# Kernel optimization log

Hardware: AMD Instinct MI355X
Metric: run time of the kernel (lower is better)

## Reference

```python
import jax, jax.numpy as jnp
import numpy as np

HIDDEN = 4096
N_HEADS = 32
N_KV_HEADS = 8
HEAD_DIM = HIDDEN // N_HEADS  # 128
N_GROUPS = N_HEADS // N_KV_HEADS  # 4
ROPE_THETA = 10000.0
BSZ, SEQ = 2, 2048


def rotate_half(x):
    x1 = x[..., : x.shape[-1] // 2]
    x2 = x[..., x.shape[-1] // 2 :]
    return jnp.concatenate((-x2, x1), axis=-1)


def rope_tables(seq_len, head_dim, theta):
    inv_freq = 1.0 / theta ** (jnp.arange(0, head_dim, 2, dtype=jnp.float32) / head_dim)
    t = jnp.arange(seq_len, dtype=jnp.float32)
    freqs = jnp.einsum('i,j->ij', t, inv_freq)          # [S, head_dim/2]
    emb = jnp.concatenate((freqs, freqs), axis=-1)       # [S, head_dim]
    return jnp.cos(emb), jnp.sin(emb)


def setup_inputs() -> dict:
    key = jax.random.key(0)
    ks = jax.random.split(key, 5)
    hidden_states = jax.random.normal(ks[0], (BSZ, SEQ, HIDDEN), dtype=jnp.float32)
    # causal additive mask [B, 1, Q, K]
    causal = jnp.tril(jnp.ones((SEQ, SEQ), dtype=bool))
    attention_mask = jnp.where(causal, 0.0, -1e9).astype(jnp.float32)
    attention_mask = jnp.broadcast_to(attention_mask[None, None], (BSZ, 1, SEQ, SEQ))
    position_ids = jnp.broadcast_to(jnp.arange(SEQ, dtype=jnp.int32)[None, :], (BSZ, SEQ))
    sc = 1.0 / np.sqrt(HIDDEN)
    Wq = jax.random.normal(ks[1], (HIDDEN, N_HEADS * HEAD_DIM), dtype=jnp.float32) * sc
    Wk = jax.random.normal(ks[2], (HIDDEN, N_KV_HEADS * HEAD_DIM), dtype=jnp.float32) * sc
    Wv = jax.random.normal(ks[3], (HIDDEN, N_KV_HEADS * HEAD_DIM), dtype=jnp.float32) * sc
    Wo = jax.random.normal(ks[4], (N_HEADS * HEAD_DIM, HIDDEN), dtype=jnp.float32) * sc
    return {
        'hidden_states': hidden_states,
        'attention_mask': attention_mask,
        'position_ids': position_ids,
        'Wq': Wq, 'Wk': Wk, 'Wv': Wv, 'Wo': Wo,
    }


def reference(hidden_states, attention_mask, position_ids, Wq, Wk, Wv, Wo):
    bsz, q_len, _ = hidden_states.shape
    # QKV projections
    q = (hidden_states @ Wq).reshape(bsz, q_len, N_HEADS, HEAD_DIM).swapaxes(1, 2)       # [B,H,S,D]
    k = (hidden_states @ Wk).reshape(bsz, q_len, N_KV_HEADS, HEAD_DIM).swapaxes(1, 2)    # [B,Hkv,S,D]
    v = (hidden_states @ Wv).reshape(bsz, q_len, N_KV_HEADS, HEAD_DIM).swapaxes(1, 2)    # [B,Hkv,S,D]
    # RoPE
    cos_t, sin_t = rope_tables(q_len, HEAD_DIM, ROPE_THETA)
    cos = jnp.take(cos_t, position_ids, axis=0)[:, None]  # [B,1,S,D]
    sin = jnp.take(sin_t, position_ids, axis=0)[:, None]
    q = q * cos + rotate_half(q) * sin
    k = k * cos + rotate_half(k) * sin
    # GQA attention via grouped einsum (equivalent to repeat_kv, without materializing repeats)
    qg = q.reshape(bsz, N_KV_HEADS, N_GROUPS, q_len, HEAD_DIM)
    scores = jnp.einsum('bhgqd,bhkd->bhgqk', qg, k) / jnp.sqrt(jnp.float32(HEAD_DIM))
    scores = scores + attention_mask[:, :, None]  # broadcast mask over (kv_head, group)
    probs = jax.nn.softmax(scores.astype(jnp.float32), axis=-1).astype(hidden_states.dtype)
    out = jnp.einsum('bhgqk,bhkd->bhgqd', probs, v)
    out = out.reshape(bsz, N_HEADS, q_len, HEAD_DIM).swapaxes(1, 2).reshape(bsz, q_len, HIDDEN)
    return out @ Wo
```

## Files before the change

kernel.cpp:

```cpp
#include <hip/hip_runtime.h>
#include <hip/hip_bf16.h>
#include <cstdint>

#define HIDDEN 4096
#define NH 32
#define NKV 8
#define HD 128
#define SEQ 2048
#define BSZ 2
#define QKVN 6144
#define QKVLD 6144

using bf16x8 = __attribute__((ext_vector_type(8))) short;
using f32x4  = __attribute__((ext_vector_type(4))) float;
using f32x16 = __attribute__((ext_vector_type(16))) float;

__device__ __forceinline__ ushort f2bf(float f) {
  union { float f; uint32_t u; } v; v.f = f;
  uint32_t r = (v.u + 0x7FFFu + ((v.u >> 16) & 1u)) >> 16;
  return (ushort)r;
}
__device__ __forceinline__ float bf2f(ushort s) {
  union { uint32_t u; float f; } v; v.u = ((uint32_t)s) << 16;
  return v.f;
}

__device__ __forceinline__ uint32_t cvtpk(float lo, float hi) {
  uint32_t r;
  asm("v_cvt_pk_bf16_f32 %0, %1, %2" : "=v"(r) : "v"(lo), "v"(hi));
  return r;
}
__device__ __forceinline__ void pl32swap(uint32_t& a, uint32_t& b) {
  asm("v_permlane32_swap_b32 %0, %1" : "+v"(a), "+v"(b));
}

__device__ __forceinline__ void gload_lds16(const void* g, void* l) {
  __builtin_amdgcn_global_load_lds(
      (const __attribute__((address_space(1))) void*)g,
      (__attribute__((address_space(3))) void*)l, 16, 0, 0);
}

__global__ __launch_bounds__(256)
void cvt_bf16_kernel(const float* __restrict__ X, ushort* __restrict__ Xb, int n8) {
  int t = blockIdx.x * 256 + threadIdx.x;
  if (t >= n8) return;
  size_t i = (size_t)t * 8;
  float4 a = *(const float4*)(X + i);
  float4 b = *(const float4*)(X + i + 4);
  uint4 p;
  p.x = (uint)f2bf(a.x) | ((uint)f2bf(a.y) << 16);
  p.y = (uint)f2bf(a.z) | ((uint)f2bf(a.w) << 16);
  p.z = (uint)f2bf(b.x) | ((uint)f2bf(b.y) << 16);
  p.w = (uint)f2bf(b.z) | ((uint)f2bf(b.w) << 16);
  *(uint4*)(Xb + i) = p;
}

__global__ __launch_bounds__(256)
void transpose_bf16_kernel(const float* __restrict__ W, ushort* __restrict__ WT,
                           int K, int N) {
  __shared__ ushort tile[64][72];
  const int k0 = blockIdx.y * 64, n0 = blockIdx.x * 64;
  const int tr = threadIdx.x >> 4;
  const int tc = (threadIdx.x & 15) * 4;
#pragma unroll
  for (int i = 0; i < 4; ++i) {
    const int k = tr + i * 16;
    float4 v = *(const float4*)(W + (size_t)(k0 + k) * N + n0 + tc);
    ushort4 u;
    u.x = f2bf(v.x); u.y = f2bf(v.y); u.z = f2bf(v.z); u.w = f2bf(v.w);
    *(ushort4*)&tile[k][tc] = u;
  }
  __syncthreads();
  const int nr = threadIdx.x >> 3;
  const int kc = (threadIdx.x & 7) * 8;
#pragma unroll
  for (int i = 0; i < 2; ++i) {
    const int n = nr + i * 32;
    bf16x8 o;
#pragma unroll
    for (int j = 0; j < 8; ++j) o[j] = tile[kc + j][n];
    *(bf16x8*)(WT + (size_t)(n0 + n) * K + k0 + kc) = o;
  }
}

__global__ __launch_bounds__(256)
void transpose_v_kernel(const ushort* __restrict__ Vsrc, ushort* __restrict__ VtG) {
  __shared__ ushort tile[64][72];
  const int slice = blockIdx.z;
  const int b = slice >> 3, kh = slice & 7;
  const int s0 = blockIdx.x * 64, d0 = blockIdx.y * 64;
  const ushort* src = Vsrc + ((size_t)(b * SEQ) + s0) * QKVLD + kh * HD + d0;
  const int sr = threadIdx.x >> 3;
  const int dc = (threadIdx.x & 7) * 8;
#pragma unroll
  for (int i = 0; i < 2; ++i) {
    const int s = sr + i * 32;
    *(bf16x8*)&tile[s][dc] = *(const bf16x8*)(src + (size_t)s * QKVLD + dc);
  }
  __syncthreads();
  ushort* dst = VtG + ((size_t)slice * HD + d0) * SEQ + s0;
  const int dr = threadIdx.x >> 3;
  const int sc = (threadIdx.x & 7) * 8;
#pragma unroll
  for (int i = 0; i < 2; ++i) {
    const int d = dr + i * 32;
    bf16x8 o;
#pragma unroll
    for (int j = 0; j < 8; ++j) o[j] = tile[sc + j][d];
    *(bf16x8*)(dst + (size_t)d * SEQ + sc) = o;
  }
}

__global__ __launch_bounds__(512, 2)
void gemmqkv_kernel(const ushort* __restrict__ A, const ushort* __restrict__ BT,
                    ushort* __restrict__ Cp, int M, int N, int K) {
  extern __shared__ ushort lds[];
  const int tid = threadIdx.x, lane = tid & 63, wave = tid >> 6;
  const int l15 = lane & 15, l4 = lane >> 4;
  const int wr = wave >> 2, wc = wave & 3;

  const int mt = M >> 8, ntile = N / 192, nwg = mt * ntile;
  const int swq = nwg >> 3, swr = nwg & 7;
  const int xcd = blockIdx.x & 7, lo = blockIdx.x >> 3;
  const int wg = (xcd < swr ? xcd * (swq + 1) : swr * (swq + 1) + (xcd - swr) * swq) + lo;
  const int m0 = (wg % mt) << 8;
  const int n0 = (wg / mt) * 192;

  ushort* LA[2][2];
  ushort* LB[2][2];
#pragma unroll
  for (int b_ = 0; b_ < 2; ++b_)
#pragma unroll
    for (int s_ = 0; s_ < 2; ++s_) {
      LA[b_][s_] = lds + (b_ * 2 + s_) * 8192;
      LB[b_][s_] = lds + 32768 + (b_ * 2 + s_) * 6144;
    }

  const ushort* Abase = A + (size_t)m0 * K;
  const ushort* Bbase = BT + (size_t)n0 * K;

  const int srow0 = tid >> 2;
  const int scol8 = (((tid & 3) ^ ((srow0 >> 1) & 3)) << 3);
  const int bs1 = tid;
  const int brow1 = bs1 >> 2;
  const int bcol1 = (((bs1 & 3) ^ ((bs1 >> 3) & 3)) << 3);
  const int bs2 = 512 + wave * 32 + (lane & 31);
  const int brow2 = bs2 >> 2;
  const int bcol2 = (((bs2 & 3) ^ ((bs2 >> 3) & 3)) << 3);

  const int swb  = (l4 ^ ((l15 >> 1) & 3)) << 3;
  const int aoff = (wr * 128 + l15) * 32 + swb;
  const int boff = (wc * 48 + l15) * 32 + swb;

  f32x4 acc[8][3] = {};
  bf16x8 a[4];
  bf16x8 b[3];

#define STAGE_EV(buf, ks, kt)                                                  \
  do {                                                                         \
    const size_t gc_ = (size_t)(kt) * 64 + (ks) * 32;                          \
    gload_lds16(Abase + (size_t)srow0 * K + gc_ + scol8,                       \
                &LA[buf][ks][tid * 8]);                                        \
    gload_lds16(Bbase + (size_t)brow1 * K + gc_ + bcol1,                       \
                &LB[buf][ks][tid * 8]);                                        \
  } while (0)

#define STAGE_OD(buf, ks, kt)                                                  \
  do {                                                                         \
    const size_t gc_ = (size_t)(kt) * 64 + (ks) * 32;                          \
    gload_lds16(Abase + (size_t)(128 + srow0) * K + gc_ + scol8,               \
                &LA[buf][ks][(512 + tid) * 8]);                                \
    if ((lane & 32) == 0)                                                      \
      gload_lds16(Bbase + (size_t)brow2 * K + gc_ + bcol2,                     \
                  &LB[buf][ks][(512 + wave * 32 + (lane & 31)) * 8]);          \
  } while (0)

#define MFMA_ __builtin_amdgcn_mfma_f32_16x16x32_bf16

#define PHASE_EVEN(buf, ks, sb, sk, skt)                                       \
  {                                                                            \
    _Pragma("unroll") for (int m_ = 0; m_ < 4; ++m_)                           \
      a[m_] = *(const bf16x8*)&LA[buf][ks][aoff + m_ * 512];                   \
    _Pragma("unroll") for (int n_ = 0; n_ < 3; ++n_)                           \
      b[n_] = *(const bf16x8*)&LB[buf][ks][boff + n_ * 512];                   \
    STAGE_EV(sb, sk, skt);                                                     \
    asm volatile("s_barrier" ::: "memory");                                    \
    __builtin_amdgcn_s_setprio(1);                                             \
    _Pragma("unroll") for (int m_ = 0; m_ < 4; ++m_)                           \
      _Pragma("unroll") for (int n_ = 0; n_ < 3; ++n_)                         \
        acc[m_][n_] = MFMA_(a[m_], b[n_], acc[m_][n_], 0, 0, 0);               \
    __builtin_amdgcn_s_setprio(0);                                             \
    asm volatile("s_barrier" ::: "memory");                                    \
  }

#define PHASE_ODD(buf, ks, sb, sk, skt)                                        \
  {                                                                            \
    _Pragma("unroll") for (int m_ = 0; m_ < 4; ++m_)                           \
      a[m_] = *(const bf16x8*)&LA[buf][ks][aoff + (4 + m_) * 512];             \
    STAGE_OD(sb, sk, skt);                                                     \
    asm volatile("s_barrier" ::: "memory");                                    \
    __builtin_amdgcn_s_setprio(1);                                             \
    _Pragma("unroll") for (int m_ = 0; m_ < 4; ++m_)                           \
      _Pragma("unroll") for (int n_ = 0; n_ < 3; ++n_)                         \
        acc[4 + m_][n_] = MFMA_(a[m_], b[n_], acc[4 + m_][n_], 0, 0, 0);       \
    __builtin_amdgcn_s_setprio(0);                                             \
    asm volatile("s_waitcnt vmcnt(8)");                                        \
    asm volatile("s_barrier" ::: "memory");                                    \
  }

  const int NT = K >> 6;

  STAGE_EV(0, 0, 0); STAGE_OD(0, 0, 0);
  STAGE_EV(0, 1, 0); STAGE_OD(0, 1, 0);
  STAGE_EV(1, 0, 1); STAGE_OD(1, 0, 1);
  asm volatile("s_waitcnt vmcnt(8)");
  asm volatile("s_barrier" ::: "memory");

  for (int i = 0; i < (NT >> 1); ++i) {
    const int kt0 = 2 * i;
    const int ktA = (kt0 + 2 < NT) ? kt0 + 2 : NT - 1;
    const int ktB = (kt0 + 3 < NT) ? kt0 + 3 : NT - 1;
    PHASE_EVEN(0, 0, 1, 1, kt0 + 1)
    PHASE_ODD (0, 0, 1, 1, kt0 + 1)
    PHASE_EVEN(0, 1, 0, 0, ktA)
    PHASE_ODD (0, 1, 0, 0, ktA)
    PHASE_EVEN(1, 0, 0, 1, ktA)
    PHASE_ODD (1, 0, 0, 1, ktA)
    PHASE_EVEN(1, 1, 1, 0, ktB)
    PHASE_ODD (1, 1, 1, 0, ktB)
  }
#undef PHASE_EVEN
#undef PHASE_ODD
#undef STAGE_EV
#undef STAGE_OD

  const int crow0 = m0 + wr * 128 + l4 * 4;
  const int ccol0 = n0 + wc * 48 + l15;
#pragma unroll
  for (int m_ = 0; m_ < 8; ++m_)
#pragma unroll
    for (int n_ = 0; n_ < 3; ++n_)
#pragma unroll
      for (int r_ = 0; r_ < 4; ++r_) {
        const size_t row = crow0 + m_ * 16 + r_;
        const int col = ccol0 + n_ * 16;
        Cp[row * N + col] = f2bf(acc[m_][n_][r_]);
      }
}

template<int OUT_BF16>
__global__ __launch_bounds__(512, 2)
void gemm8p_kernel(const ushort* __restrict__ A, const ushort* __restrict__ BT,
                   void* __restrict__ Cp, int M, int N, int K) {
  extern __shared__ ushort lds[];
  const int tid = threadIdx.x, lane = tid & 63, wave = tid >> 6;
  const int l15 = lane & 15, l4 = lane >> 4;
  const int wr = wave >> 2, wc = wave & 3;

  const int mt = M >> 8, nt = N >> 8, nwg = mt * nt;
  const int swq = nwg >> 3, swr = nwg & 7;
  const int xcd = blockIdx.x & 7, lo = blockIdx.x >> 3;
  const int wg = (xcd < swr ? xcd * (swq + 1) : swr * (swq + 1) + (xcd - swr) * swq) + lo;
  const int m0 = (wg % mt) << 8;
  const int n0 = (wg / mt) << 8;

  ushort* LA[2][2];
  ushort* LB[2][2];
#pragma unroll
  for (int b_ = 0; b_ < 2; ++b_)
#pragma unroll
    for (int s_ = 0; s_ < 2; ++s_) {
      LA[b_][s_] = lds + ((b_ * 2 + 0) * 2 + s_) * 8192;
      LB[b_][s_] = lds + ((b_ * 2 + 1) * 2 + s_) * 8192;
    }

  const ushort* Abase = A + (size_t)m0 * K;
  const ushort* Bbase = BT + (size_t)n0 * K;

  const int srow0 = tid >> 2;
  const int scol8 = (((tid & 3) ^ ((srow0 >> 1) & 3)) << 3);

  const int swb  = (l4 ^ ((l15 >> 1) & 3)) << 3;
  const int aoff = (wr * 128 + l15) * 32 + swb;
  const int boff = (wc * 64 + l15) * 32 + swb;

  f32x4 acc[8][4] = {};
  bf16x8 a[8];
  bf16x8 b[4];

#define STAGE(buf, ks, kt, part)                                              \
  do {                                                                        \
    const size_t gc_ = (size_t)(kt) * 64 + (ks) * 32 + scol8;                 \
    const int rw_ = srow0 + (part) * 128;                                     \
    const int dst_ = ((part) * 512 + tid) * 8;                                \
    gload_lds16(Abase + (size_t)rw_ * K + gc_, &LA[buf][ks][dst_]);           \
    gload_lds16(Bbase + (size_t)rw_ * K + gc_, &LB[buf][ks][dst_]);           \
  } while (0)

#define MFMA_ __builtin_amdgcn_mfma_f32_16x16x32_bf16

#define PHASE_EVEN(buf, ks, sb, sk, skt)                                      \
  {                                                                           \
    _Pragma("unroll") for (int m_ = 0; m_ < 8; ++m_)                          \
      a[m_] = *(const bf16x8*)&LA[buf][ks][aoff + m_ * 512];                  \
    b[0] = *(const bf16x8*)&LB[buf][ks][boff];                                \
    b[1] = *(const bf16x8*)&LB[buf][ks][boff + 512];                          \
    STAGE(sb, sk, skt, 0);                                                    \
    asm volatile("s_barrier" ::: "memory");                                   \
    __builtin_amdgcn_s_setprio(1);                                            \
    _Pragma("unroll") for (int m_ = 0; m_ < 8; ++m_) {                        \
      acc[m_][0] = MFMA_(a[m_], b[0], acc[m_][0], 0, 0, 0);                   \
      acc[m_][1] = MFMA_(a[m_], b[1], acc[m_][1], 0, 0, 0);                   \
    }                                                                         \
    __builtin_amdgcn_s_setprio(0);                                            \
    asm volatile("s_barrier" ::: "memory");                                   \
  }

#define PHASE_ODD(buf, ks, sb, sk, skt)                                       \
  {                                                                           \
    b[2] = *(const bf16x8*)&LB[buf][ks][boff + 1024];                         \
    b[3] = *(const bf16x8*)&LB[buf][ks][boff + 1536];                         \
    STAGE(sb, sk, skt, 1);                                                    \
    asm volatile("s_barrier" ::: "memory");                                   \
    __builtin_amdgcn_s_setprio(1);                                            \
    _Pragma("unroll") for (int m_ = 0; m_ < 8; ++m_) {                        \
      acc[m_][2] = MFMA_(a[m_], b[2], acc[m_][2], 0, 0, 0);                   \
      acc[m_][3] = MFMA_(a[m_], b[3], acc[m_][3], 0, 0, 0);                   \
    }                                                                         \
    __builtin_amdgcn_s_setprio(0);                                            \
    asm volatile("s_waitcnt vmcnt(8)");                                       \
    asm volatile("s_barrier" ::: "memory");                                   \
  }

  const int NT = K >> 6;

  STAGE(0, 0, 0, 0); STAGE(0, 0, 0, 1);
  STAGE(0, 1, 0, 0); STAGE(0, 1, 0, 1);
  STAGE(1, 0, 1, 0); STAGE(1, 0, 1, 1);
  asm volatile("s_waitcnt vmcnt(8)");
  asm volatile("s_barrier" ::: "memory");

  for (int i = 0; i < (NT >> 1); ++i) {
    const int kt0 = 2 * i;
    const int ktA = (kt0 + 2 < NT) ? kt0 + 2 : NT - 1;
    const int ktB = (kt0 + 3 < NT) ? kt0 + 3 : NT - 1;
    PHASE_EVEN(0, 0, 1, 1, kt0 + 1)
    PHASE_ODD (0, 0, 1, 1, kt0 + 1)
    PHASE_EVEN(0, 1, 0, 0, ktA)
    PHASE_ODD (0, 1, 0, 0, ktA)
    PHASE_EVEN(1, 0, 0, 1, ktA)
    PHASE_ODD (1, 0, 0, 1, ktA)
    PHASE_EVEN(1, 1, 1, 0, ktB)
    PHASE_ODD (1, 1, 1, 0, ktB)
  }
#undef PHASE_EVEN
#undef PHASE_ODD
#undef STAGE

  const int crow0 = m0 + wr * 128 + l4 * 4;
  const int ccol0 = n0 + wc * 64 + l15;
#pragma unroll
  for (int m_ = 0; m_ < 8; ++m_)
#pragma unroll
    for (int n_ = 0; n_ < 4; ++n_)
#pragma unroll
      for (int r_ = 0; r_ < 4; ++r_) {
        const size_t row = crow0 + m_ * 16 + r_;
        const int col = ccol0 + n_ * 16;
        const float val = acc[m_][n_][r_];
        if (OUT_BF16) ((ushort*)Cp)[row * N + col] = f2bf(val);
        else          ((float*)Cp)[row * N + col]  = val;
      }
}

__global__ __launch_bounds__(256)
void rope_qk_kernel(ushort* qkv, const int* __restrict__ pos_ids, int total) {
  int t = blockIdx.x * 256 + threadIdx.x;
  if (t >= total) return;
  int j = t & 63;
  int rest = t >> 6;
  int hp = rest % 40;
  int bs = rest / 40;
  float pos = (float)pos_ids[bs];
  float inv = exp2f(-(float)j * (13.287712379549449f / 64.0f));
  float ang = pos * inv;
  const float osc = (hp < 32) ? 0.12751731f : 1.0f;
  float c = cosf(ang) * osc, s = sinf(ang) * osc;
  const int col = (hp < 32) ? hp * HD : HIDDEN + (hp - 32) * HD;
  ushort* p = qkv + (size_t)bs * QKVLD + col + j;
  float x1 = bf2f(p[0]), x2 = bf2f(p[64]);
  p[0]  = f2bf(x1 * c - x2 * s);
  p[64] = f2bf(x2 * c + x1 * s);
}

__global__ __launch_bounds__(512)
void attn_kernel(const ushort* __restrict__ Q, const ushort* __restrict__ K0,
                 const ushort* __restrict__ VtG, ushort* __restrict__ AO) {
  __shared__ ushort Ks[64 * 128];
  __shared__ ushort Vs[2][128 * 64];

  const int bid = blockIdx.x;
  const int kh  = bid & 7;
  const int r2  = bid >> 3;
  const int qtB = 7 - (r2 & 7);
  const int hq  = (r2 >> 3) & 3;
  const int b   = r2 >> 5;
  const int h   = kh * 4 + hq;
  const int q0b = qtB * 256;

  const int tid = threadIdx.x, lane = tid & 63, w = tid >> 6;
  const int l31 = lane & 31, hi = lane >> 5;
  const int q0w = q0b + w * 32;

  const size_t bS = (size_t)b * SEQ;
  const ushort* Kb = K0 + bS * QKVLD + kh * HD;
  const ushort* Vb = VtG + (size_t)(b * NKV + kh) * HD * SEQ;

  bf16x8 qf[8];
  {
    const ushort* qp = Q + (bS + q0w + l31) * QKVLD + h * HD + hi * 8;
#pragma unroll
    for (int ds = 0; ds < 8; ++ds) qf[ds] = *(const bf16x8*)(qp + ds * 16);
  }

  f32x16 accO[4] = {};
  float mrow = -1e30f, denom = 0.0f;

  const int nt = qtB * 4 + 4;

  const int j0 = 2 * w, j1 = 2 * w + 1;
  const int kl4 = lane >> 4, ks15 = lane & 15;
  const int vl3 = lane >> 3, vs7 = lane & 7;
  const int kswz = lane & 15;
  const int vswz = lane & 7;

#define KSTAGE(jj, kk0) { const int k_ = (jj) * 4 + kl4;                       \
    gload_lds16(Kb + (size_t)((kk0) + k_) * QKVLD + ((ks15 ^ (k_ & 15)) << 3), \
                &Ks[(jj) * 512 + lane * 8]); }
#define VSTAGE(jj, bb, kk0) { const int d_ = (jj) * 8 + vl3;                   \
    gload_lds16(Vb + (size_t)d_ * SEQ + (kk0) + ((vs7 ^ (d_ & 7)) << 3),       \
                &Vs[bb][(jj) * 512 + lane * 8]); }

  KSTAGE(j0, 0) KSTAGE(j1, 0) VSTAGE(j0, 0, 0) VSTAGE(j1, 0, 0)
  __syncthreads();

  for (int t = 0; t < nt; ++t) {
    const int k0 = t * 64;
    const int cur = t & 1;
    const bool pf = (t + 1 < nt);
    const bool skip = (k0 > q0w + 31);

    f32x16 s0 = {}, s1 = {};
    if (!skip) {
      __builtin_amdgcn_s_setprio(1);
#pragma unroll
      for (int ds = 0; ds < 8; ++ds) {
        const int so = ((ds * 2 + hi) ^ kswz) << 3;
        bf16x8 kf0 = *(const bf16x8*)&Ks[l31 * 128 + so];
        bf16x8 kf1 = *(const bf16x8*)&Ks[(32 + l31) * 128 + so];
        s0 = __builtin_amdgcn_mfma_f32_32x32x16_bf16(kf0, qf[ds], s0, 0, 0, 0);
        s1 = __builtin_amdgcn_mfma_f32_32x32x16_bf16(kf1, qf[ds], s1, 0, 0, 0);
      }
      __builtin_amdgcn_s_setprio(0);
    }
    __syncthreads();

    if (pf) {
      const int kn = k0 + 64;
      KSTAGE(j0, kn) KSTAGE(j1, kn) VSTAGE(j0, cur ^ 1, kn) VSTAGE(j1, cur ^ 1, kn)
    }

    if (!skip) {
      if (k0 + 63 > q0w) {
        const int qrel = q0w + l31 - k0;
#pragma unroll
        for (int r = 0; r < 16; ++r) {
          const int kc = (r & 3) + 8 * (r >> 2) + 4 * hi;
          if (kc > qrel)      s0[r] = -1e30f;
          if (kc + 32 > qrel) s1[r] = -1e30f;
        }
      }
      float pm = s0[0];
#pragma unroll
      for (int r = 1; r < 16; ++r) pm = fmaxf(pm, s0[r]);
#pragma unroll
      for (int r = 0; r < 16; ++r) pm = fmaxf(pm, s1[r]);

      if (!__all(pm - mrow <= 8.0f)) {
        pm = fmaxf(pm, __shfl_xor(pm, 32));
        const float mn = fmaxf(mrow, pm);
        const float alpha = exp2f(mrow - mn);
        mrow = mn;
        denom *= alpha;
#pragma unroll
        for (int du = 0; du < 4; ++du)
#pragma unroll
          for (int r = 0; r < 16; ++r) accO[du][r] *= alpha;
      }
      float ssum = 0.0f;
#pragma unroll
      for (int r = 0; r < 16; ++r) { float p = exp2f(s0[r] - mrow); s0[r] = p; ssum += p; }
#pragma unroll
      for (int r = 0; r < 16; ++r) { float p = exp2f(s1[r] - mrow); s1[r] = p; ssum += p; }
      denom += ssum;

      uint32_t paw[4][4];
      {
        uint32_t p0 = cvtpk(s0[0], s0[1]),   p1 = cvtpk(s0[2], s0[3]);
        uint32_t p2 = cvtpk(s0[4], s0[5]),   p3 = cvtpk(s0[6], s0[7]);
        uint32_t p4 = cvtpk(s0[8], s0[9]),   p5 = cvtpk(s0[10], s0[11]);
        uint32_t p6 = cvtpk(s0[12], s0[13]), p7 = cvtpk(s0[14], s0[15]);
        pl32swap(p0, p2); pl32swap(p1, p3); pl32swap(p4, p6); pl32swap(p5, p7);
        paw[0][0] = p0; paw[0][1] = p1; paw[0][2] = p2; paw[0][3] = p3;
        paw[1][0] = p4; paw[1][1] = p5; paw[1][2] = p6; paw[1][3] = p7;
      }
      {
        uint32_t p0 = cvtpk(s1[0], s1[1]),   p1 = cvtpk(s1[2], s1[3]);
        uint32_t p2 = cvtpk(s1[4], s1[5]),   p3 = cvtpk(s1[6], s1[7]);
        uint32_t p4 = cvtpk(s1[8], s1[9]),   p5 = cvtpk(s1[10], s1[11]);
        uint32_t p6 = cvtpk(s1[12], s1[13]), p7 = cvtpk(s1[14], s1[15]);
        pl32swap(p0, p2); pl32swap(p1, p3); pl32swap(p4, p6); pl32swap(p5, p7);
        paw[2][0] = p0; paw[2][1] = p1; paw[2][2] = p2; paw[2][3] = p3;
        paw[3][0] = p4; paw[3][1] = p5; paw[3][2] = p6; paw[3][3] = p7;
      }

      __builtin_amdgcn_s_setprio(1);
#pragma unroll
      for (int du = 0; du < 4; ++du) {
#pragma unroll
        for (int ks = 0; ks < 4; ++ks) {
          const int so = ((ks * 2 + hi) ^ vswz) << 3;
          bf16x8 vf = *(const bf16x8*)&Vs[cur][(du * 32 + l31) * 64 + so];
          bf16x8 pb = *(const bf16x8*)&paw[ks][0];
          accO[du] = __builtin_amdgcn_mfma_f32_32x32x16_bf16(vf, pb, accO[du], 0, 0, 0);
        }
      }
      __builtin_amdgcn_s_setprio(0);
    }
    __syncthreads();
  }
#undef KSTAGE
#undef VSTAGE

  denom += __shfl_xor(denom, 32);
  const float inv = 1.0f / denom;
  ushort* op = AO + (bS + q0w + l31) * HIDDEN + h * HD + hi * 4;
#pragma unroll
  for (int du = 0; du < 4; ++du)
#pragma unroll
    for (int g = 0; g < 4; ++g) {
      uint2 u;
      u.x = cvtpk(accO[du][4 * g + 0] * inv, accO[du][4 * g + 1] * inv);
      u.y = cvtpk(accO[du][4 * g + 2] * inv, accO[du][4 * g + 3] * inv);
      *(uint2*)(op + du * 32 + g * 8) = u;
    }
}

extern "C" void kernel_launch(void* const* d_in, const int* in_sizes, int n_in,
                              void* d_out, int out_size, void* d_ws, size_t ws_size,
                              hipStream_t stream) {
  (void)in_sizes; (void)n_in; (void)out_size; (void)ws_size;
  const float* X   = (const float*)d_in[0];
  const int*   pos = (const int*)d_in[2];
  const float* Wq  = (const float*)d_in[3];
  const float* Wk  = (const float*)d_in[4];
  const float* Wv  = (const float*)d_in[5];
  const float* Wo  = (const float*)d_in[6];

  char* ws = (char*)d_ws;
  ushort* Xb    = (ushort*)(ws);
  ushort* QKV   = (ushort*)(ws + 33554432);
  ushort* BTqkv = (ushort*)(ws + 83886080);
  ushort* WoT   = (ushort*)(ws + 134217728);
  ushort* AO    = Xb;
  ushort* VtG   = BTqkv;

  const int M = BSZ * SEQ;
  dim3 blk(256);

  hipFuncSetAttribute((const void*)gemmqkv_kernel,
                      hipFuncAttributeMaxDynamicSharedMemorySize, 114688);
  hipFuncSetAttribute((const void*)gemm8p_kernel<0>,
                      hipFuncAttributeMaxDynamicSharedMemorySize, 131072);

  cvt_bf16_kernel<<<dim3((M * HIDDEN / 8 + 255) / 256), blk, 0, stream>>>(X, Xb, M * HIDDEN / 8);
  transpose_bf16_kernel<<<dim3(HIDDEN / 64, HIDDEN / 64), blk, 0, stream>>>(Wq, BTqkv, HIDDEN, HIDDEN);
  transpose_bf16_kernel<<<dim3((NKV * HD) / 64, HIDDEN / 64), blk, 0, stream>>>(
      Wk, BTqkv + (size_t)HIDDEN * HIDDEN, HIDDEN, NKV * HD);
  transpose_bf16_kernel<<<dim3((NKV * HD) / 64, HIDDEN / 64), blk, 0, stream>>>(
      Wv, BTqkv + (size_t)(HIDDEN + NKV * HD) * HIDDEN, HIDDEN, NKV * HD);
  transpose_bf16_kernel<<<dim3(HIDDEN / 64, HIDDEN / 64), blk, 0, stream>>>(Wo, WoT, HIDDEN, HIDDEN);

  gemmqkv_kernel<<<dim3((M / 256) * (QKVN / 192)), dim3(512), 114688, stream>>>(
      Xb, BTqkv, QKV, M, QKVN, HIDDEN);

  rope_qk_kernel<<<dim3((M * 40 * 64) / 256), blk, 0, stream>>>(QKV, pos, M * 40 * 64);
  transpose_v_kernel<<<dim3(SEQ / 64, HD / 64, BSZ * NKV), blk, 0, stream>>>(
      QKV + HIDDEN + NKV * HD, VtG);

  attn_kernel<<<dim3(512), dim3(512), 0, stream>>>(QKV, QKV + HIDDEN, VtG, AO);

  gemm8p_kernel<0><<<dim3((M / 256) * (HIDDEN / 256)), dim3(512), 131072, stream>>>(
      AO, WoT, d_out, M, HIDDEN, HIDDEN);
}
```

Measured before the change: 575.0 us.

## Double-buffer K tiles in attention and rebalance GEMM fragment loads per phase

The attention kernel now double-buffers the K tile in shared memory, the same way V already was. This lets the next K/V prefetch be issued at the start of each iteration, before the QK^T MFMAs, and removes the __syncthreads that sat between the score computation and the prefetch. Separately, the GEMM main loop now loads 4 A and 4 B fragments in the even phase and the remaining 4 A fragments in the odd phase, instead of 8 A plus 2 B then 2 more B. This lowers register use for A fragments and spreads LDS reads more evenly across the two phases. Doubling the K buffer adds 16 KB of LDS per block, which may reduce occupancy. Removing the barrier also depends on the remaining synchronisation in the cut code being enough to avoid races.

```diff
diff --git a/kernel.cpp b/kernel.cpp
--- a/kernel.cpp
+++ b/kernel.cpp
@@ -285,7 +285,7 @@
   const int boff = (wc * 64 + l15) * 32 + swb;
 
   f32x4 acc[8][4] = {};
-  bf16x8 a[8];
+  bf16x8 a[4];
   bf16x8 b[4];
 
 #define STAGE(buf, ks, kt, part)                                              \
@@ -301,32 +301,30 @@
 
 #define PHASE_EVEN(buf, ks, sb, sk, skt)                                      \
   {                                                                           \
-    _Pragma("unroll") for (int m_ = 0; m_ < 8; ++m_)                          \
+    _Pragma("unroll") for (int m_ = 0; m_ < 4; ++m_)                          \
       a[m_] = *(const bf16x8*)&LA[buf][ks][aoff + m_ * 512];                  \
-    b[0] = *(const bf16x8*)&LB[buf][ks][boff];                                \
-    b[1] = *(const bf16x8*)&LB[buf][ks][boff + 512];                          \
+    _Pragma("unroll") for (int n_ = 0; n_ < 4; ++n_)                          \
+      b[n_] = *(const bf16x8*)&LB[buf][ks][boff + n_ * 512];                  \
     STAGE(sb, sk, skt, 0);                                                    \
     asm volatile("s_barrier" ::: "memory");                                   \
     __builtin_amdgcn_s_setprio(1);                                            \
-    _Pragma("unroll") for (int m_ = 0; m_ < 8; ++m_) {                        \
-      acc[m_][0] = MFMA_(a[m_], b[0], acc[m_][0], 0, 0, 0);                   \
-      acc[m_][1] = MFMA_(a[m_], b[1], acc[m_][1], 0, 0, 0);                   \
-    }                                                                         \
+    _Pragma("unroll") for (int m_ = 0; m_ < 4; ++m_)                          \
+      _Pragma("unroll") for (int n_ = 0; n_ < 4; ++n_)                        \
+        acc[m_][n_] = MFMA_(a[m_], b[n_], acc[m_][n_], 0, 0, 0);              \
     __builtin_amdgcn_s_setprio(0);                                            \
     asm volatile("s_barrier" ::: "memory");                                   \
   }
 
 #define PHASE_ODD(buf, ks, sb, sk, skt)                                       \
   {                                                                           \
-    b[2] = *(const bf16x8*)&LB[buf][ks][boff + 1024];                         \
-    b[3] = *(const bf16x8*)&LB[buf][ks][boff + 1536];                         \
+    _Pragma("unroll") for (int m_ = 0; m_ < 4; ++m_)                          \
+      a[m_] = *(const bf16x8*)&LA[buf][ks][aoff + (4 + m_) * 512];            \
     STAGE(sb, sk, skt, 1);                                                    \
     asm volatile("s_barrier" ::: "memory");                                   \
     __builtin_amdgcn_s_setprio(1);                                            \
-    _Pragma("unroll") for (int m_ = 0; m_ < 8; ++m_) {                        \
-      acc[m_][2] = MFMA_(a[m_], b[2], acc[m_][2], 0, 0, 0);                   \
-      acc[m_][3] = MFMA_(a[m_], b[3], acc[m_][3], 0, 0, 0);                   \
-    }                                                                         \
+    _Pragma("unroll") for (int m_ = 0; m_ < 4; ++m_)                          \
+      _Pragma("unroll") for (int n_ = 0; n_ < 4; ++n_)                        \
+        acc[4 + m_][n_] = MFMA_(a[m_], b[n_], acc[4 + m_][n_], 0, 0, 0);      \
     __builtin_amdgcn_s_setprio(0);                                            \
     asm volatile("s_waitcnt vmcnt(8)");                                       \
     asm volatile("s_barrier" ::: "memory");                                   \
@@ -396,7 +394,7 @@
 __global__ __launch_bounds__(512)
 void attn_kernel(const ushort* __restrict__ Q, const ushort* __restrict__ K0,
                  const ushort* __restrict__ VtG, ushort* __restrict__ AO) {
-  __shared__ ushort Ks[64 * 128];
+  __shared__ ushort Ks[2][64 * 128];
   __shared__ ushort Vs[2][128 * 64];
 
   const int bid = blockIdx.x;
@@ -434,14 +432,14 @@
   const int kswz = lane & 15;
   const int vswz = lane & 7;
 
-#define KSTAGE(jj, kk0) { const int k_ = (jj) * 4 + kl4;                       \
+#define KSTAGE(jj, bb, kk0) { const int k_ = (jj) * 4 + kl4;                   \
     gload_lds16(Kb + (size_t)((kk0) + k_) * QKVLD + ((ks15 ^ (k_ & 15)) << 3), \
-                &Ks[(jj) * 512 + lane * 8]); }
+                &Ks[bb][(jj) * 512 + lane * 8]); }
 #define VSTAGE(jj, bb, kk0) { const int d_ = (jj) * 8 + vl3;                   \
     gload_lds16(Vb + (size_t)d_ * SEQ + (kk0) + ((vs7 ^ (d_ & 7)) << 3),       \
                 &Vs[bb][(jj) * 512 + lane * 8]); }
 
-  KSTAGE(j0, 0) KSTAGE(j1, 0) VSTAGE(j0, 0, 0) VSTAGE(j1, 0, 0)
+  KSTAGE(j0, 0, 0) KSTAGE(j1, 0, 0) VSTAGE(j0, 0, 0) VSTAGE(j1, 0, 0)
   __syncthreads();
 
   for (int t = 0; t < nt; ++t) {
@@ -450,27 +448,25 @@
     const bool pf = (t + 1 < nt);
     const bool skip = (k0 > q0w + 31);
 
-    f32x16 s0 = {}, s1 = {};
+    if (pf) {
+      const int kn = k0 + 64;
+      KSTAGE(j0, cur ^ 1, kn) KSTAGE(j1, cur ^ 1, kn)
+      VSTAGE(j0, cur ^ 1, kn) VSTAGE(j1, cur ^ 1, kn)
+    }
+
     if (!skip) {
+      f32x16 s0 = {}, s1 = {};
       __builtin_amdgcn_s_setprio(1);
 #pragma unroll
       for (int ds = 0; ds < 8; ++ds) {
         const int so = ((ds * 2 + hi) ^ kswz) << 3;
-        bf16x8 kf0 = *(const bf16x8*)&Ks[l31 * 128 + so];
-        bf16x8 kf1 = *(const bf16x8*)&Ks[(32 + l31) * 128 + so];
+        bf16x8 kf0 = *(const bf16x8*)&Ks[cur][l31 * 128 + so];
+        bf16x8 kf1 = *(const bf16x8*)&Ks[cur][(32 + l31) * 128 + so];
         s0 = __builtin_amdgcn_mfma_f32_32x32x16_bf16(kf0, qf[ds], s0, 0, 0, 0);
         s1 = __builtin_amdgcn_mfma_f32_32x32x16_bf16(kf1, qf[ds], s1, 0, 0, 0);
       }
       __builtin_amdgcn_s_setprio(0);
-    }
-    __syncthreads();
-
-    if (pf) {
-      const int kn = k0 + 64;
-      KSTAGE(j0, kn) KSTAGE(j1, kn) VSTAGE(j0, cur ^ 1, kn) VSTAGE(j1, cur ^ 1, kn)
-    }
-
-    if (!skip) {
+
       if (k0 + 63 > q0w) {
         const int qrel = q0w + l31 - k0;
 #pragma unroll
```

Result: no change. 583.3 us (+1.5%).

## Deepen attention K/V prefetch to a four-buffer ring and fuse weight transposes

Applied to the files above, without the earlier changes.

The attention kernel now uses 128 KB of dynamic shared memory as a four-slot ring for K and V tiles. It prefetches two tiles ahead and processes two key tiles per loop iteration, so it needs one barrier per pair of tiles instead of two per tile. The four separate weight transpose/convert launches are merged into one kernel that picks its source matrix from the block index. The larger LDS footprint may cut attention blocks resident per CU, trading occupancy for deeper memory overlap.

```diff
diff --git a/kernel.cpp b/kernel.cpp
--- a/kernel.cpp
+++ b/kernel.cpp
@@ -56,10 +56,20 @@
 }
 
 __global__ __launch_bounds__(256)
-void transpose_bf16_kernel(const float* __restrict__ W, ushort* __restrict__ WT,
-                           int K, int N) {
+void transpose_all_kernel(const float* __restrict__ Wq, const float* __restrict__ Wk,
+                          const float* __restrict__ Wv, const float* __restrict__ Wo,
+                          ushort* __restrict__ BTqkv, ushort* __restrict__ WoT) {
   __shared__ ushort tile[64][72];
-  const int k0 = blockIdx.y * 64, n0 = blockIdx.x * 64;
+  const int id = blockIdx.x;
+  const float* W; ushort* WT; int N, rel;
+  if (id < 4096)      { W = Wq; WT = BTqkv;                          N = 4096; rel = id; }
+  else if (id < 5120) { W = Wk; WT = BTqkv + (size_t)4096 * 4096;    N = 1024; rel = id - 4096; }
+  else if (id < 6144) { W = Wv; WT = BTqkv + (size_t)5120 * 4096;    N = 1024; rel = id - 5120; }
+  else                { W = Wo; WT = WoT;                            N = 4096; rel = id - 6144; }
+  const int K = 4096;
+  const int nb = N >> 6;
+  const int n0 = (rel % nb) * 64, k0 = (rel / nb) * 64;
+
   const int tr = threadIdx.x >> 4;
   const int tc = (threadIdx.x & 15) * 4;
 #pragma unroll
@@ -396,8 +406,14 @@
 __global__ __launch_bounds__(512)
 void attn_kernel(const ushort* __restrict__ Q, const ushort* __restrict__ K0,
                  const ushort* __restrict__ VtG, ushort* __restrict__ AO) {
-  __shared__ ushort Ks[64 * 128];
-  __shared__ ushort Vs[2][128 * 64];
+  extern __shared__ ushort alds[];
+  ushort* Ks[4];
+  ushort* Vs[4];
+#pragma unroll
+  for (int i = 0; i < 4; ++i) {
+    Ks[i] = alds + i * 8192;
+    Vs[i] = alds + 32768 + i * 8192;
+  }
 
   const int bid = blockIdx.x;
   const int kh  = bid & 7;
@@ -434,43 +450,46 @@
   const int kswz = lane & 15;
   const int vswz = lane & 7;
 
-#define KSTAGE(jj, kk0) { const int k_ = (jj) * 4 + kl4;                       \
+#define KSTAGE(jj, bb, kk0) { const int k_ = (jj) * 4 + kl4;                   \
     gload_lds16(Kb + (size_t)((kk0) + k_) * QKVLD + ((ks15 ^ (k_ & 15)) << 3), \
-                &Ks[(jj) * 512 + lane * 8]); }
+                &Ks[bb][(jj) * 512 + lane * 8]); }
 #define VSTAGE(jj, bb, kk0) { const int d_ = (jj) * 8 + vl3;                   \
     gload_lds16(Vb + (size_t)d_ * SEQ + (kk0) + ((vs7 ^ (d_ & 7)) << 3),       \
                 &Vs[bb][(jj) * 512 + lane * 8]); }
 
-  KSTAGE(j0, 0) KSTAGE(j1, 0) VSTAGE(j0, 0, 0) VSTAGE(j1, 0, 0)
+  KSTAGE(j0, 0, 0)  KSTAGE(j1, 0, 0)  VSTAGE(j0, 0, 0)  VSTAGE(j1, 0, 0)
+  KSTAGE(j0, 1, 64) KSTAGE(j1, 1, 64) VSTAGE(j0, 1, 64) VSTAGE(j1, 1, 64)
   __syncthreads();
 
-  for (int t = 0; t < nt; ++t) {
-    const int k0 = t * 64;
-    const int cur = t & 1;
-    const bool pf = (t + 1 < nt);
-    const bool skip = (k0 > q0w + 31);
-
-    f32x16 s0 = {}, s1 = {};
-    if (!skip) {
+  for (int t = 0; t < nt; t += 2) {
+    if (t + 2 < nt) {
+      const int bb = (t + 2) & 3, kk = (t + 2) * 64;
+      KSTAGE(j0, bb, kk) KSTAGE(j1, bb, kk) VSTAGE(j0, bb, kk) VSTAGE(j1, bb, kk)
+    }
+    if (t + 3 < nt) {
+      const int bb = (t + 3) & 3, kk = (t + 3) * 64;
+      KSTAGE(j0, bb, kk) KSTAGE(j1, bb, kk) VSTAGE(j0, bb, kk) VSTAGE(j1, bb, kk)
+    }
+
+#pragma unroll
+    for (int u = 0; u < 2; ++u) {
+      const int tt = t + u;
+      const int k0 = tt * 64;
+      const int cb = tt & 3;
+      if (k0 > q0w + 31) continue;
+
+      f32x16 s0 = {}, s1 = {};
       __builtin_amdgcn_s_setprio(1);
 #pragma unroll
       for (int ds = 0; ds < 8; ++ds) {
         const int so = ((ds * 2 + hi) ^ kswz) << 3;
-        bf16x8 kf0 = *(const bf16x8*)&Ks[l31 * 128 + so];
-        bf16x8 kf1 = *(const bf16x8*)&Ks[(32 + l31) * 128 + so];
+        bf16x8 kf0 = *(const bf16x8*)&Ks[cb][l31 * 128 + so];
+        bf16x8 kf1 = *(const bf16x8*)&Ks[cb][(32 + l31) * 128 + so];
         s0 = __builtin_amdgcn_mfma_f32_32x32x16_bf16(kf0, qf[ds], s0, 0, 0, 0);
         s1 = __builtin_amdgcn_mfma_f32_32x32x16_bf16(kf1, qf[ds], s1, 0, 0, 0);
       }
       __builtin_amdgcn_s_setprio(0);
-    }
-    __syncthreads();
-
-    if (pf) {
-      const int kn = k0 + 64;
-      KSTAGE(j0, kn) KSTAGE(j1, kn) VSTAGE(j0, cur ^ 1, kn) VSTAGE(j1, cur ^ 1, kn)
-    }
-
-    if (!skip) {
+
       if (k0 + 63 > q0w) {
         const int qrel = q0w + l31 - k0;
 #pragma unroll
@@ -530,7 +549,7 @@
 #pragma unroll
         for (int ks = 0; ks < 4; ++ks) {
           const int so = ((ks * 2 + hi) ^ vswz) << 3;
-          bf16x8 vf = *(const bf16x8*)&Vs[cur][(du * 32 + l31) * 64 + so];
+          bf16x8 vf = *(const bf16x8*)&Vs[cb][(du * 32 + l31) * 64 + so];
           bf16x8 pb = *(const bf16x8*)&paw[ks][0];
           accO[du] = __builtin_amdgcn_mfma_f32_32x32x16_bf16(vf, pb, accO[du], 0, 0, 0);
         }
@@ -582,14 +601,11 @@
                       hipFuncAttributeMaxDynamicSharedMemorySize, 114688);
   hipFuncSetAttribute((const void*)gemm8p_kernel<0>,
                       hipFuncAttributeMaxDynamicSharedMemorySize, 131072);
+  hipFuncSetAttribute((const void*)attn_kernel,
+                      hipFuncAttributeMaxDynamicSharedMemorySize, 131072);
 
   cvt_bf16_kernel<<<dim3((M * HIDDEN / 8 + 255) / 256), blk, 0, stream>>>(X, Xb, M * HIDDEN / 8);
-  transpose_bf16_kernel<<<dim3(HIDDEN / 64, HIDDEN / 64), blk, 0, stream>>>(Wq, BTqkv, HIDDEN, HIDDEN);
-  transpose_bf16_kernel<<<dim3((NKV * HD) / 64, HIDDEN / 64), blk, 0, stream>>>(
-      Wk, BTqkv + (size_t)HIDDEN * HIDDEN, HIDDEN, NKV * HD);
-  transpose_bf16_kernel<<<dim3((NKV * HD) / 64, HIDDEN / 64), blk, 0, stream>>>(
-      Wv, BTqkv + (size_t)(HIDDEN + NKV * HD) * HIDDEN, HIDDEN, NKV * HD);
-  transpose_bf16_kernel<<<dim3(HIDDEN / 64, HIDDEN / 64), blk, 0, stream>>>(Wo, WoT, HIDDEN, HIDDEN);
+  transpose_all_kernel<<<dim3(10240), blk, 0, stream>>>(Wq, Wk, Wv, Wo, BTqkv, WoT);
 
   gemmqkv_kernel<<<dim3((M / 256) * (QKVN / 192)), dim3(512), 114688, stream>>>(
       Xb, BTqkv, QKV, M, QKVN, HIDDEN);
@@ -598,7 +614,7 @@
   transpose_v_kernel<<<dim3(SEQ / 64, HD / 64, BSZ * NKV), blk, 0, stream>>>(
       QKV + HIDDEN + NKV * HD, VtG);
 
-  attn_kernel<<<dim3(512), dim3(512), 0, stream>>>(QKV, QKV + HIDDEN, VtG, AO);
+  attn_kernel<<<dim3(512), dim3(512), 131072, stream>>>(QKV, QKV + HIDDEN, VtG, AO);
 
   gemm8p_kernel<0><<<dim3((M / 256) * (HIDDEN / 256)), dim3(512), 131072, stream>>>(
       AO, WoT, d_out, M, HIDDEN, HIDDEN);
```

Result: no change. 569.6 us (median of 3 runs) (-0.9%).
